# Kernel tuning notes

Measured on AMD Instinct MI355X. Metric: run time of the kernel, lower is better.

Reference implementation:

```python
import jax, jax.numpy as jnp
import numpy as np

B, T, D, H = 4, 2048, 1024, 16
DK = D // H

def setup_inputs() -> dict:
    key = jax.random.key(0)
    k1, k2, k3 = jax.random.split(key, 3)
    x = jax.random.normal(k1, (B, T, D), dtype=jnp.float32)
    w_qkv = jax.random.normal(k2, (D, 3 * D), dtype=jnp.float32) * (1.0 / np.sqrt(D))
    w_proj = jax.random.normal(k3, (D, D), dtype=jnp.float32) * (1.0 / np.sqrt(D))
    # additive causal mask: 0 on/below diagonal, -inf above
    neg = jnp.finfo(jnp.float32).min
    attn_mask = jnp.where(jnp.tril(jnp.ones((T, T), dtype=bool)), 0.0, neg)[None, None]
    return {"x": x, "attn_mask": attn_mask, "w_qkv": w_qkv, "w_proj": w_proj}


def reference(x, attn_mask, w_qkv, w_proj):
    Bx, Tx, Dx = x.shape
    qkv = x @ w_qkv                                  # [B,T,3D]
    q, k, v = jnp.split(qkv, 3, axis=-1)
    # [B,T,D] -> [B,H,T,dk]
    def to_heads(t):
        return t.reshape(Bx, Tx, H, DK).transpose(0, 2, 1, 3)
    q, k, v = to_heads(q), to_heads(k), to_heads(v)
    attn = jnp.einsum("bhqd,bhkd->bhqk", q, k) / jnp.sqrt(jnp.float32(DK))
    attn = attn + attn_mask
    attn = jax.nn.softmax(attn, axis=-1)
    out = jnp.einsum("bhqk,bhkd->bhqd", attn, v)     # [B,H,T,dk]
    out = out.transpose(0, 2, 1, 3).reshape(Bx, Tx, Dx)
    return out @ w_proj
```

## Files before the change

### kernel.cpp

```cpp
#include <hip/hip_runtime.h>
#include <hip/hip_bf16.h>
#include <stdint.h>

typedef __bf16 bf16x8 __attribute__((ext_vector_type(8)));
typedef __bf16 bf16x4 __attribute__((ext_vector_type(4)));
typedef float  f32x4  __attribute__((ext_vector_type(4)));

__device__ __forceinline__ void gl_lds16(const void* g, void* l) {
  __builtin_amdgcn_global_load_lds(
      (const __attribute__((address_space(1))) unsigned int*)g,
      (__attribute__((address_space(3))) unsigned int*)l, 16, 0, 0);
}

__global__ __launch_bounds__(256) void prep_kernel(
    const float* __restrict__ x, __bf16* __restrict__ Xb,
    const float* __restrict__ w_qkv, __bf16* __restrict__ wt_qkv,
    const float* __restrict__ w_proj, __bf16* __restrict__ wt_proj) {
  __shared__ __bf16 tile[64][65];
  const int bid = blockIdx.x, t = threadIdx.x;
  if (bid < 4096) {
    const size_t i = ((size_t)bid * 256 + t) * 8;
    float4 v0 = *reinterpret_cast<const float4*>(x + i);
    float4 v1 = *reinterpret_cast<const float4*>(x + i + 4);
    bf16x8 o;
    o[0] = (__bf16)v0.x; o[1] = (__bf16)v0.y; o[2] = (__bf16)v0.z; o[3] = (__bf16)v0.w;
    o[4] = (__bf16)v1.x; o[5] = (__bf16)v1.y; o[6] = (__bf16)v1.z; o[7] = (__bf16)v1.w;
    *reinterpret_cast<bf16x8*>(Xb + i) = o;
    return;
  }
  const float* src; __bf16* dst; int K, N, bx, by;
  if (bid < 4864) {
    int idx = bid - 4096;
    src = w_qkv; dst = wt_qkv; K = 1024; N = 3072;
    bx = idx % 48; by = idx / 48;
  } else {
    int idx = bid - 4864;
    src = w_proj; dst = wt_proj; K = 1024; N = 1024;
    bx = idx & 15; by = idx >> 4;
  }
  const int n0 = bx * 64, k0 = by * 64;
#pragma unroll
  for (int e = 0; e < 16; ++e) {
    int idx = e * 256 + t;
    int kk = idx >> 6, nn = idx & 63;
    tile[nn][kk] = (__bf16)src[(size_t)(k0 + kk) * N + n0 + nn];
  }
  __syncthreads();
#pragma unroll
  for (int e = 0; e < 16; ++e) {
    int idx = e * 256 + t;
    int nn = idx >> 6, kk = idx & 63;
    dst[(size_t)(n0 + nn) * K + k0 + kk] = tile[nn][kk];
  }
}

template <int NFRAG>
__device__ __forceinline__ void gemm_core_1024(
    const __bf16* __restrict__ Ag, const __bf16* __restrict__ Bg,
    int m0, int n0, __bf16* lds, f32x4 (&acc)[8][NFRAG]) {
  constexpr int BUFSZ = 4096 + NFRAG * 2048;
  const int tid = threadIdx.x;
  const int wv = tid >> 6, l = tid & 63, g = l >> 4, lr = l & 15;
  const int sswL = (lr & 3) ^ ((lr >> 2) & 3);

  int arow[2], acol[2], brow[NFRAG], bcol[NFRAG];
#pragma unroll
  for (int e = 0; e < 2; ++e) {
    int c = e * 256 + tid, row = c >> 2, slot = c & 3;
    arow[e] = row;
    acol[e] = (slot ^ ((row & 3) ^ ((row >> 2) & 3))) * 8;
  }
#pragma unroll
  for (int e = 0; e < NFRAG; ++e) {
    int c = e * 256 + tid, row = c >> 2, slot = c & 3;
    brow[e] = row;
    bcol[e] = (slot ^ ((row & 3) ^ ((row >> 2) & 3))) * 8;
  }

  auto STAGE = [&](int bufb, int t) {
    const int kb = t * 32;
#pragma unroll
    for (int e = 0; e < 2; ++e)
      gl_lds16(Ag + (size_t)(m0 + arow[e]) * 1024 + kb + acol[e],
               lds + bufb + (e * 256 + wv * 64) * 8);
#pragma unroll
    for (int e = 0; e < NFRAG; ++e)
      gl_lds16(Bg + (size_t)(n0 + brow[e]) * 1024 + kb + bcol[e],
               lds + bufb + 4096 + (e * 256 + wv * 64) * 8);
  };

  int cur = 0, nx = BUFSZ, nn = 2 * BUFSZ;
  STAGE(cur, 0);
  STAGE(nx, 1);

#pragma unroll 1
  for (int t = 0; t < 32; ++t) {
    if (t < 31) {
      if constexpr (NFRAG == 3) asm volatile("s_waitcnt vmcnt(5)" ::: "memory");
      else                      asm volatile("s_waitcnt vmcnt(4)" ::: "memory");
    } else {
      asm volatile("s_waitcnt vmcnt(0)" ::: "memory");
    }
    __builtin_amdgcn_s_barrier();
    __builtin_amdgcn_sched_barrier(0);
    if (t + 2 < 32) STAGE(nn, t + 2);

    const char* Ab = (const char*)(lds + cur);
    const char* Bb = (const char*)(lds + cur + 4096);
    bf16x8 a[8], b[NFRAG];
#pragma unroll
    for (int mf = 0; mf < 8; ++mf)
      a[mf] = *reinterpret_cast<const bf16x8*>(
          Ab + (mf * 16 + lr) * 64 + ((g ^ sswL) << 4));
#pragma unroll
    for (int nf = 0; nf < NFRAG; ++nf)
      b[nf] = *reinterpret_cast<const bf16x8*>(
          Bb + (wv * NFRAG * 16 + nf * 16 + lr) * 64 + ((g ^ sswL) << 4));
    __builtin_amdgcn_s_setprio(1);
#pragma unroll
    for (int mf = 0; mf < 8; ++mf)
#pragma unroll
      for (int nf = 0; nf < NFRAG; ++nf)
        acc[mf][nf] = __builtin_amdgcn_mfma_f32_16x16x32_bf16(
            a[mf], b[nf], acc[mf][nf], 0, 0, 0);
    __builtin_amdgcn_s_setprio(0);

    int tmp = cur; cur = nx; nx = nn; nn = tmp;
  }
}

__global__ __launch_bounds__(256, 2) void qkv_gemm(
    const __bf16* __restrict__ Xb, const __bf16* __restrict__ WT,
    __bf16* __restrict__ Qb, __bf16* __restrict__ Kb, __bf16* __restrict__ Vb) {
  __shared__ __bf16 lds[30720];
  const int lin = blockIdx.x;
  const int sw = (lin & 7) * 128 + (lin >> 3);
  const int rb = sw >> 4, cb = sw & 15;
  const int m0 = rb * 128, n0 = cb * 192;

  f32x4 acc[8][3] = {};
  gemm_core_1024<3>(Xb, WT, m0, n0, lds, acc);

  const int tid = threadIdx.x, wv = tid >> 6, l = tid & 63, g = l >> 4, lr = l & 15;
#pragma unroll
  for (int mf = 0; mf < 8; ++mf)
#pragma unroll
    for (int nf = 0; nf < 3; ++nf) {
      int m_ = m0 + mf * 16 + g * 4;
      int nb = n0 + wv * 48 + nf * 16;
      int which = nb >> 10, hc = nb & 1023;
      int hh = hc >> 6, dk0 = hc & 63;
      int bbv = m_ >> 11, tt = m_ & 2047;
      if (which == 2) {
        bf16x4 vk;
        vk[0] = (__bf16)acc[mf][nf][0]; vk[1] = (__bf16)acc[mf][nf][1];
        vk[2] = (__bf16)acc[mf][nf][2]; vk[3] = (__bf16)acc[mf][nf][3];
        *reinterpret_cast<bf16x4*>(
            &Vb[((size_t)(bbv * 16 + hh) * 64 + dk0 + lr) * 2048 + tt]) = vk;
      } else if (which == 0) {
#pragma unroll
        for (int j = 0; j < 4; ++j)
          Qb[(((size_t)(bbv * 16 + hh)) * 2048 + tt + j) * 64 + dk0 + lr] =
              (__bf16)(acc[mf][nf][j] * 0.18033688f);
      } else {
#pragma unroll
        for (int j = 0; j < 4; ++j)
          Kb[(((size_t)(bbv * 16 + hh)) * 2048 + tt + j) * 64 + dk0 + lr] =
              (__bf16)acc[mf][nf][j];
      }
    }
}

__global__ __launch_bounds__(256, 2) void proj_gemm(
    const __bf16* __restrict__ A, const __bf16* __restrict__ WT,
    float* __restrict__ Out) {
  __shared__ __bf16 lds[24576];
  const int lin = blockIdx.x;
  const int sw = (lin & 7) * 64 + (lin >> 3);
  const int rb = sw >> 3, cb = sw & 7;
  const int m0 = rb * 128, n0 = cb * 128;

  f32x4 acc[8][2] = {};
  gemm_core_1024<2>(A, WT, m0, n0, lds, acc);

  const int tid = threadIdx.x, wv = tid >> 6, l = tid & 63, g = l >> 4, lr = l & 15;
#pragma unroll
  for (int mf = 0; mf < 8; ++mf)
#pragma unroll
    for (int nf = 0; nf < 2; ++nf) {
      int m_ = m0 + mf * 16 + g * 4;
      int n  = n0 + wv * 32 + nf * 16 + lr;
#pragma unroll
      for (int j = 0; j < 4; ++j)
        Out[(size_t)(m_ + j) * 1024 + n] = acc[mf][nf][j];
    }
}

__global__ __launch_bounds__(256, 2) void attn_kernel(
    const __bf16* __restrict__ Qb, const __bf16* __restrict__ Kb,
    const __bf16* __restrict__ VTb, __bf16* __restrict__ Ob) {
  __shared__ __bf16 Ks[2][4096];
  __shared__ __bf16 Vs[2][4096];
  __shared__ __bf16 PlA[4][1024];
  __shared__ __bf16 PlB[4][1024];
  const int t = threadIdx.x, l = t & 63, w = t >> 6;
  const int g = l >> 4, lr = l & 15;
  const int bid = blockIdx.x;
  const int logical = (bid & 7) * 64 + (bid >> 3);
  const int pj = logical & 7, bh = logical >> 3;
  const int bb = bh >> 4, h = bh & 15;
  const __bf16* Kbase = Kb  + (size_t)bh * 2048 * 64;
  const __bf16* Vbase = VTb + (size_t)bh * 64 * 2048;
  const __bf16* Qbase = Qb  + (size_t)bh * 2048 * 64;
  const int swz = (lr & 7) << 4;

  int cur = 0;
#pragma unroll 1
  for (int phase = 0; phase < 2; ++phase) {
    const int J = phase ? (15 - pj) : pj;
    const int qtA = 2 * J, qtB = 2 * J + 1;
    const int qrowA = J * 128 + w * 16 + lr;
    const int qrowB = qrowA + 64;
    const bf16x8 qfA0 = *reinterpret_cast<const bf16x8*>(Qbase + (size_t)qrowA * 64 + g * 8);
    const bf16x8 qfA1 = *reinterpret_cast<const bf16x8*>(Qbase + (size_t)qrowA * 64 + 32 + g * 8);
    const bf16x8 qfB0 = *reinterpret_cast<const bf16x8*>(Qbase + (size_t)qrowB * 64 + g * 8);
    const bf16x8 qfB1 = *reinterpret_cast<const bf16x8*>(Qbase + (size_t)qrowB * 64 + 32 + g * 8);

    f32x4 otA[4] = {}, otB[4] = {};
    float lsA = 0.f, lsB = 0.f;

#pragma unroll
    for (int rep = 0; rep < 2; ++rep) {
      int c = w * 128 + rep * 64 + l;
      int row = c >> 3, cc = c & 7;
      int pc = (cc ^ (row & 7)) * 8;
      gl_lds16(Kbase + (size_t)row * 64 + pc, &Ks[cur][(w * 128 + rep * 64) * 8]);
      gl_lds16(Vbase + (size_t)row * 2048 + pc, &Vs[cur][(w * 128 + rep * 64) * 8]);
    }
    __syncthreads();

    for (int kt = 0; kt <= qtB; ++kt) {
      const bool aAct = (kt <= qtA);
      if (kt < qtB) {
        const int nv0 = (kt + 1) * 64;
#pragma unroll
        for (int rep = 0; rep < 2; ++rep) {
          int c = w * 128 + rep * 64 + l;
          int row = c >> 3, cc = c & 7;
          int pc = (cc ^ (row & 7)) * 8;
          gl_lds16(Kbase + (size_t)(nv0 + row) * 64 + pc,
                   &Ks[cur ^ 1][(w * 128 + rep * 64) * 8]);
          gl_lds16(Vbase + (size_t)row * 2048 + nv0 + pc,
                   &Vs[cur ^ 1][(w * 128 + rep * 64) * 8]);
        }
      }
      bf16x8 klo[4], khi[4];
#pragma unroll
      for (int nf = 0; nf < 4; ++nf) {
        const char* kr = (const char*)&Ks[cur][(nf * 16 + lr) * 64];
        klo[nf] = *reinterpret_cast<const bf16x8*>(kr + ((g * 16) ^ swz));
        khi[nf] = *reinterpret_cast<const bf16x8*>(kr + ((64 + g * 16) ^ swz));
      }
      f32x4 stA[4], stB[4];
      __builtin_amdgcn_s_setprio(1);
#pragma unroll
      for (int nf = 0; nf < 4; ++nf) {
        f32x4 z = {};
        z = __builtin_amdgcn_mfma_f32_16x16x32_bf16(klo[nf], qfB0, z, 0, 0, 0);
        stB[nf] = __builtin_amdgcn_mfma_f32_16x16x32_bf16(khi[nf], qfB1, z, 0, 0, 0);
      }
      if (aAct) {
#pragma unroll
        for (int nf = 0; nf < 4; ++nf) {
          f32x4 z = {};
          z = __builtin_amdgcn_mfma_f32_16x16x32_bf16(klo[nf], qfA0, z, 0, 0, 0);
          stA[nf] = __builtin_amdgcn_mfma_f32_16x16x32_bf16(khi[nf], qfA1, z, 0, 0, 0);
        }
      }
      __builtin_amdgcn_s_setprio(0);
      if (kt == qtB) {
#pragma unroll
        for (int nf = 0; nf < 4; ++nf)
#pragma unroll
          for (int j = 0; j < 4; ++j)
            if (nf * 16 + g * 4 + j > w * 16 + lr) stB[nf][j] = -INFINITY;
      }
      if (aAct && kt == qtA) {
#pragma unroll
        for (int nf = 0; nf < 4; ++nf)
#pragma unroll
          for (int j = 0; j < 4; ++j)
            if (nf * 16 + g * 4 + j > w * 16 + lr) stA[nf][j] = -INFINITY;
      }
      {
        float rs = 0.f;
        char* prow = (char*)&PlB[w][lr * 64];
#pragma unroll
        for (int nf = 0; nf < 4; ++nf) {
#pragma unroll
          for (int j = 0; j < 4; ++j) {
            float p = __builtin_amdgcn_exp2f(stB[nf][j]);
            stB[nf][j] = p;
            rs += p;
          }
          bf16x4 pk;
          pk[0] = (__bf16)stB[nf][0]; pk[1] = (__bf16)stB[nf][1];
          pk[2] = (__bf16)stB[nf][2]; pk[3] = (__bf16)stB[nf][3];
          *reinterpret_cast<bf16x4*>(prow + ((nf * 32 + g * 8) ^ swz)) = pk;
        }
        lsB += rs;
      }
      if (aAct) {
        float rs = 0.f;
        char* prow = (char*)&PlA[w][lr * 64];
#pragma unroll
        for (int nf = 0; nf < 4; ++nf) {
#pragma unroll
          for (int j = 0; j < 4; ++j) {
            float p = __builtin_amdgcn_exp2f(stA[nf][j]);
            stA[nf][j] = p;
            rs += p;
          }
          bf16x4 pk;
          pk[0] = (__bf16)stA[nf][0]; pk[1] = (__bf16)stA[nf][1];
          pk[2] = (__bf16)stA[nf][2]; pk[3] = (__bf16)stA[nf][3];
          *reinterpret_cast<bf16x4*>(prow + ((nf * 32 + g * 8) ^ swz)) = pk;
        }
        lsA += rs;
      }
      {
        bf16x8 vlo[4], vhi[4];
#pragma unroll
        for (int nf = 0; nf < 4; ++nf) {
          const char* vr = (const char*)&Vs[cur][(nf * 16 + lr) * 64];
          vlo[nf] = *reinterpret_cast<const bf16x8*>(vr + ((g * 16) ^ swz));
          vhi[nf] = *reinterpret_cast<const bf16x8*>(vr + ((64 + g * 16) ^ swz));
        }
        const char* prB = (const char*)&PlB[w][lr * 64];
        bf16x8 pb0 = *reinterpret_cast<const bf16x8*>(prB + ((g * 16) ^ swz));
        bf16x8 pb1 = *reinterpret_cast<const bf16x8*>(prB + ((64 + g * 16) ^ swz));
        __builtin_amdgcn_s_setprio(1);
#pragma unroll
        for (int nf = 0; nf < 4; ++nf) {
          otB[nf] = __builtin_amdgcn_mfma_f32_16x16x32_bf16(vlo[nf], pb0, otB[nf], 0, 0, 0);
          otB[nf] = __builtin_amdgcn_mfma_f32_16x16x32_bf16(vhi[nf], pb1, otB[nf], 0, 0, 0);
        }
        __builtin_amdgcn_s_setprio(0);
        if (aAct) {
          const char* prA = (const char*)&PlA[w][lr * 64];
          bf16x8 pa0 = *reinterpret_cast<const bf16x8*>(prA + ((g * 16) ^ swz));
          bf16x8 pa1 = *reinterpret_cast<const bf16x8*>(prA + ((64 + g * 16) ^ swz));
          __builtin_amdgcn_s_setprio(1);
#pragma unroll
          for (int nf = 0; nf < 4; ++nf) {
            otA[nf] = __builtin_amdgcn_mfma_f32_16x16x32_bf16(vlo[nf], pa0, otA[nf], 0, 0, 0);
            otA[nf] = __builtin_amdgcn_mfma_f32_16x16x32_bf16(vhi[nf], pa1, otA[nf], 0, 0, 0);
          }
          __builtin_amdgcn_s_setprio(0);
        }
      }
      __syncthreads();
      cur ^= 1;
    }

    lsA += __shfl_xor(lsA, 16); lsA += __shfl_xor(lsA, 32);
    lsB += __shfl_xor(lsB, 16); lsB += __shfl_xor(lsB, 32);
    const float rlA = 1.f / lsA, rlB = 1.f / lsB;
#pragma unroll
    for (int nf = 0; nf < 4; ++nf) {
      bf16x4 ok;
      ok[0] = (__bf16)(otA[nf][0] * rlA); ok[1] = (__bf16)(otA[nf][1] * rlA);
      ok[2] = (__bf16)(otA[nf][2] * rlA); ok[3] = (__bf16)(otA[nf][3] * rlA);
      *reinterpret_cast<bf16x4*>(
          &Ob[((size_t)(bb * 2048 + qrowA)) * 1024 + h * 64 + nf * 16 + g * 4]) = ok;
      bf16x4 ok2;
      ok2[0] = (__bf16)(otB[nf][0] * rlB); ok2[1] = (__bf16)(otB[nf][1] * rlB);
      ok2[2] = (__bf16)(otB[nf][2] * rlB); ok2[3] = (__bf16)(otB[nf][3] * rlB);
      *reinterpret_cast<bf16x4*>(
          &Ob[((size_t)(bb * 2048 + qrowB)) * 1024 + h * 64 + nf * 16 + g * 4]) = ok2;
    }
  }
}

extern "C" void kernel_launch(void* const* d_in, const int* in_sizes, int n_in,
                              void* d_out, int out_size, void* d_ws, size_t ws_size,
                              hipStream_t stream) {
  const float* x      = (const float*)d_in[0];
  const float* w_qkv  = (const float*)d_in[2];
  const float* w_proj = (const float*)d_in[3];
  float* out = (float*)d_out;

  char* ws = (char*)d_ws;
  __bf16* wt_qkv  = (__bf16*)(ws);
  __bf16* wt_proj = (__bf16*)(ws + 6291456);
  __bf16* Qb      = (__bf16*)(ws + 8388608);
  __bf16* Kb      = (__bf16*)(ws + 8388608 + 16777216);
  __bf16* VTb     = (__bf16*)(ws + 8388608 + 2 * 16777216);
  __bf16* Ob      = (__bf16*)(ws + 8388608 + 3 * 16777216);
  __bf16* Xb      = Ob;

  prep_kernel<<<5120, 256, 0, stream>>>(x, Xb, w_qkv, wt_qkv, w_proj, wt_proj);
  qkv_gemm<<<1024, 256, 0, stream>>>(Xb, wt_qkv, Qb, Kb, VTb);
  attn_kernel<<<512, 256, 0, stream>>>(Qb, Kb, VTb, Ob);
  proj_gemm<<<512, 256, 0, stream>>>(Ob, wt_proj, out);
}
```

Baseline: 159.6 us.

## Switch attention to 32x32x16 MFMA and keep P in registers via lane shuffles

Rewrites the attention inner loop so each wave owns 32 query rows and uses 32x32x16 bf16 MFMA tiles instead of 16x16x32, which removes the split into A/B query halves. The softmax probabilities are repacked in registers with cross-half lane shuffles to form the B operand of the PV matmul, so the LDS round-trip and the P shared buffers are gone. It also drops the per-half inactive-tile skipping, so some fully masked work in the diagonal tile is now computed. Register pressure rises with the 16-wide accumulators.

```diff
diff --git a/kernel.cpp b/kernel.cpp
--- a/kernel.cpp
+++ b/kernel.cpp
@@ -5,11 +5,18 @@
 typedef __bf16 bf16x8 __attribute__((ext_vector_type(8)));
 typedef __bf16 bf16x4 __attribute__((ext_vector_type(4)));
 typedef float  f32x4  __attribute__((ext_vector_type(4)));
+typedef float  f32x16 __attribute__((ext_vector_type(16)));
 
 __device__ __forceinline__ void gl_lds16(const void* g, void* l) {
   __builtin_amdgcn_global_load_lds(
       (const __attribute__((address_space(1))) unsigned int*)g,
       (__attribute__((address_space(3))) unsigned int*)l, 16, 0, 0);
+}
+
+__device__ __forceinline__ unsigned pk2(float a, float b) {
+  union { __bf16 h[2]; unsigned u; } z;
+  z.h[0] = (__bf16)a; z.h[1] = (__bf16)b;
+  return z.u;
 }
 
 __global__ __launch_bounds__(256) void prep_kernel(
@@ -201,10 +208,8 @@
     const __bf16* __restrict__ VTb, __bf16* __restrict__ Ob) {
   __shared__ __bf16 Ks[2][4096];
   __shared__ __bf16 Vs[2][4096];
-  __shared__ __bf16 PlA[4][1024];
-  __shared__ __bf16 PlB[4][1024];
   const int t = threadIdx.x, l = t & 63, w = t >> 6;
-  const int g = l >> 4, lr = l & 15;
+  const int q5 = l & 31, hi = l >> 5;
   const int bid = blockIdx.x;
   const int logical = (bid & 7) * 64 + (bid >> 3);
   const int pj = logical & 7, bh = logical >> 3;
@@ -212,173 +217,140 @@
   const __bf16* Kbase = Kb  + (size_t)bh * 2048 * 64;
   const __bf16* Vbase = VTb + (size_t)bh * 64 * 2048;
   const __bf16* Qbase = Qb  + (size_t)bh * 2048 * 64;
-  const int swz = (lr & 7) << 4;
+
+  auto STAGEKV = [&](int buf, int kt) {
+#pragma unroll
+    for (int rep = 0; rep < 2; ++rep) {
+      int c = w * 128 + rep * 64 + l;
+      int row = c >> 3, cc = c & 7;
+      int pc = (cc ^ (row & 7)) * 8;
+      gl_lds16(Kbase + (size_t)(kt * 64 + row) * 64 + pc,
+               &Ks[buf][(w * 128 + rep * 64) * 8]);
+      gl_lds16(Vbase + (size_t)row * 2048 + kt * 64 + pc,
+               &Vs[buf][(w * 128 + rep * 64) * 8]);
+    }
+  };
 
   int cur = 0;
 #pragma unroll 1
   for (int phase = 0; phase < 2; ++phase) {
     const int J = phase ? (15 - pj) : pj;
-    const int qtA = 2 * J, qtB = 2 * J + 1;
-    const int qrowA = J * 128 + w * 16 + lr;
-    const int qrowB = qrowA + 64;
-    const bf16x8 qfA0 = *reinterpret_cast<const bf16x8*>(Qbase + (size_t)qrowA * 64 + g * 8);
-    const bf16x8 qfA1 = *reinterpret_cast<const bf16x8*>(Qbase + (size_t)qrowA * 64 + 32 + g * 8);
-    const bf16x8 qfB0 = *reinterpret_cast<const bf16x8*>(Qbase + (size_t)qrowB * 64 + g * 8);
-    const bf16x8 qfB1 = *reinterpret_cast<const bf16x8*>(Qbase + (size_t)qrowB * 64 + 32 + g * 8);
-
-    f32x4 otA[4] = {}, otB[4] = {};
-    float lsA = 0.f, lsB = 0.f;
-
-#pragma unroll
-    for (int rep = 0; rep < 2; ++rep) {
-      int c = w * 128 + rep * 64 + l;
-      int row = c >> 3, cc = c & 7;
-      int pc = (cc ^ (row & 7)) * 8;
-      gl_lds16(Kbase + (size_t)row * 64 + pc, &Ks[cur][(w * 128 + rep * 64) * 8]);
-      gl_lds16(Vbase + (size_t)row * 2048 + pc, &Vs[cur][(w * 128 + rep * 64) * 8]);
-    }
+    const int qloc = w * 32 + q5;
+    const int qrow = J * 128 + qloc;
+
+    bf16x8 qf[4];
+#pragma unroll
+    for (int ks = 0; ks < 4; ++ks)
+      qf[ks] = *reinterpret_cast<const bf16x8*>(
+          Qbase + (size_t)qrow * 64 + ks * 16 + hi * 8);
+
+    f32x16 ot[2] = {};
+    float lsum = 0.f;
+
+    STAGEKV(cur, 0);
     __syncthreads();
 
-    for (int kt = 0; kt <= qtB; ++kt) {
-      const bool aAct = (kt <= qtA);
-      if (kt < qtB) {
-        const int nv0 = (kt + 1) * 64;
-#pragma unroll
-        for (int rep = 0; rep < 2; ++rep) {
-          int c = w * 128 + rep * 64 + l;
-          int row = c >> 3, cc = c & 7;
-          int pc = (cc ^ (row & 7)) * 8;
-          gl_lds16(Kbase + (size_t)(nv0 + row) * 64 + pc,
-                   &Ks[cur ^ 1][(w * 128 + rep * 64) * 8]);
-          gl_lds16(Vbase + (size_t)row * 2048 + nv0 + pc,
-                   &Vs[cur ^ 1][(w * 128 + rep * 64) * 8]);
-        }
-      }
-      bf16x8 klo[4], khi[4];
-#pragma unroll
-      for (int nf = 0; nf < 4; ++nf) {
-        const char* kr = (const char*)&Ks[cur][(nf * 16 + lr) * 64];
-        klo[nf] = *reinterpret_cast<const bf16x8*>(kr + ((g * 16) ^ swz));
-        khi[nf] = *reinterpret_cast<const bf16x8*>(kr + ((64 + g * 16) ^ swz));
-      }
-      f32x4 stA[4], stB[4];
-      __builtin_amdgcn_s_setprio(1);
-#pragma unroll
-      for (int nf = 0; nf < 4; ++nf) {
-        f32x4 z = {};
-        z = __builtin_amdgcn_mfma_f32_16x16x32_bf16(klo[nf], qfB0, z, 0, 0, 0);
-        stB[nf] = __builtin_amdgcn_mfma_f32_16x16x32_bf16(khi[nf], qfB1, z, 0, 0, 0);
-      }
-      if (aAct) {
-#pragma unroll
-        for (int nf = 0; nf < 4; ++nf) {
-          f32x4 z = {};
-          z = __builtin_amdgcn_mfma_f32_16x16x32_bf16(klo[nf], qfA0, z, 0, 0, 0);
-          stA[nf] = __builtin_amdgcn_mfma_f32_16x16x32_bf16(khi[nf], qfA1, z, 0, 0, 0);
-        }
-      }
-      __builtin_amdgcn_s_setprio(0);
-      if (kt == qtB) {
-#pragma unroll
-        for (int nf = 0; nf < 4; ++nf)
-#pragma unroll
-          for (int j = 0; j < 4; ++j)
-            if (nf * 16 + g * 4 + j > w * 16 + lr) stB[nf][j] = -INFINITY;
-      }
-      if (aAct && kt == qtA) {
-#pragma unroll
-        for (int nf = 0; nf < 4; ++nf)
-#pragma unroll
-          for (int j = 0; j < 4; ++j)
-            if (nf * 16 + g * 4 + j > w * 16 + lr) stA[nf][j] = -INFINITY;
-      }
+    const int NT = 2 * J + 2;
+    for (int kt = 0; kt < NT; ++kt) {
+      if (kt + 1 < NT) STAGEKV(cur ^ 1, kt + 1);
+
+      f32x16 s[2] = {};
       {
-        float rs = 0.f;
-        char* prow = (char*)&PlB[w][lr * 64];
-#pragma unroll
-        for (int nf = 0; nf < 4; ++nf) {
-#pragma unroll
-          for (int j = 0; j < 4; ++j) {
-            float p = __builtin_amdgcn_exp2f(stB[nf][j]);
-            stB[nf][j] = p;
-            rs += p;
-          }
-          bf16x4 pk;
-          pk[0] = (__bf16)stB[nf][0]; pk[1] = (__bf16)stB[nf][1];
-          pk[2] = (__bf16)stB[nf][2]; pk[3] = (__bf16)stB[nf][3];
-          *reinterpret_cast<bf16x4*>(prow + ((nf * 32 + g * 8) ^ swz)) = pk;
-        }
-        lsB += rs;
-      }
-      if (aAct) {
-        float rs = 0.f;
-        char* prow = (char*)&PlA[w][lr * 64];
-#pragma unroll
-        for (int nf = 0; nf < 4; ++nf) {
-#pragma unroll
-          for (int j = 0; j < 4; ++j) {
-            float p = __builtin_amdgcn_exp2f(stA[nf][j]);
-            stA[nf][j] = p;
-            rs += p;
-          }
-          bf16x4 pk;
-          pk[0] = (__bf16)stA[nf][0]; pk[1] = (__bf16)stA[nf][1];
-          pk[2] = (__bf16)stA[nf][2]; pk[3] = (__bf16)stA[nf][3];
-          *reinterpret_cast<bf16x4*>(prow + ((nf * 32 + g * 8) ^ swz)) = pk;
-        }
-        lsA += rs;
-      }
+        const char* kr0 = (const char*)&Ks[cur][q5 * 64];
+        const char* kr1 = (const char*)&Ks[cur][(32 + q5) * 64];
+        const int sz = (q5 & 7) << 4;
+        __builtin_amdgcn_s_setprio(1);
+#pragma unroll
+        for (int ks = 0; ks < 4; ++ks) {
+          bf16x8 kf0 = *reinterpret_cast<const bf16x8*>(kr0 + ((ks * 32 + hi * 16) ^ sz));
+          bf16x8 kf1 = *reinterpret_cast<const bf16x8*>(kr1 + ((ks * 32 + hi * 16) ^ sz));
+          s[0] = __builtin_amdgcn_mfma_f32_32x32x16_bf16(kf0, qf[ks], s[0], 0, 0, 0);
+          s[1] = __builtin_amdgcn_mfma_f32_32x32x16_bf16(kf1, qf[ks], s[1], 0, 0, 0);
+        }
+        __builtin_amdgcn_s_setprio(0);
+      }
+
+      if (kt >= 2 * J) {
+        const int doff = (kt - 2 * J) * 64;
+#pragma unroll
+        for (int r = 0; r < 16; ++r) {
+          int kvloc = (r & 3) + 8 * (r >> 2) + 4 * hi;
+          if (doff + kvloc > qloc)      s[0][r] = -INFINITY;
+          if (doff + 32 + kvloc > qloc) s[1][r] = -INFINITY;
+        }
+      }
+      float rs = 0.f;
+#pragma unroll
+      for (int kvb = 0; kvb < 2; ++kvb)
+#pragma unroll
+        for (int r = 0; r < 16; ++r) {
+          float p = __builtin_amdgcn_exp2f(s[kvb][r]);
+          s[kvb][r] = p;
+          rs += p;
+        }
+      lsum += rs;
+
+      bf16x8 pb[4];
+#pragma unroll
+      for (int k = 0; k < 4; ++k) {
+        const int rb = (k & 1) * 8;
+        float o0, o1, o2, o3, e0, e1, e2, e3;
+        if (k < 2) {
+          o0 = s[0][rb + 4 * hi + 0]; o1 = s[0][rb + 4 * hi + 1];
+          o2 = s[0][rb + 4 * hi + 2]; o3 = s[0][rb + 4 * hi + 3];
+          e0 = s[0][rb + 4 * (1 - hi) + 0]; e1 = s[0][rb + 4 * (1 - hi) + 1];
+          e2 = s[0][rb + 4 * (1 - hi) + 2]; e3 = s[0][rb + 4 * (1 - hi) + 3];
+        } else {
+          o0 = s[1][rb + 4 * hi + 0]; o1 = s[1][rb + 4 * hi + 1];
+          o2 = s[1][rb + 4 * hi + 2]; o3 = s[1][rb + 4 * hi + 3];
+          e0 = s[1][rb + 4 * (1 - hi) + 0]; e1 = s[1][rb + 4 * (1 - hi) + 1];
+          e2 = s[1][rb + 4 * (1 - hi) + 2]; e3 = s[1][rb + 4 * (1 - hi) + 3];
+        }
+        unsigned ownA = pk2(o0, o1), ownB = pk2(o2, o3);
+        unsigned sndA = pk2(e0, e1), sndB = pk2(e2, e3);
+        unsigned gA = (unsigned)__shfl_xor((int)sndA, 32);
+        unsigned gB = (unsigned)__shfl_xor((int)sndB, 32);
+        union { unsigned u[4]; bf16x8 v; } z;
+        z.u[0] = hi ? gA : ownA;
+        z.u[1] = hi ? gB : ownB;
+        z.u[2] = hi ? ownA : gA;
+        z.u[3] = hi ? ownB : gB;
+        pb[k] = z.v;
+      }
+
       {
-        bf16x8 vlo[4], vhi[4];
-#pragma unroll
-        for (int nf = 0; nf < 4; ++nf) {
-          const char* vr = (const char*)&Vs[cur][(nf * 16 + lr) * 64];
-          vlo[nf] = *reinterpret_cast<const bf16x8*>(vr + ((g * 16) ^ swz));
-          vhi[nf] = *reinterpret_cast<const bf16x8*>(vr + ((64 + g * 16) ^ swz));
-        }
-        const char* prB = (const char*)&PlB[w][lr * 64];
-        bf16x8 pb0 = *reinterpret_cast<const bf16x8*>(prB + ((g * 16) ^ swz));
-        bf16x8 pb1 = *reinterpret_cast<const bf16x8*>(prB + ((64 + g * 16) ^ swz));
+        const char* vr0 = (const char*)&Vs[cur][q5 * 64];
+        const char* vr1 = (const char*)&Vs[cur][(32 + q5) * 64];
+        const int sz = (q5 & 7) << 4;
         __builtin_amdgcn_s_setprio(1);
 #pragma unroll
-        for (int nf = 0; nf < 4; ++nf) {
-          otB[nf] = __builtin_amdgcn_mfma_f32_16x16x32_bf16(vlo[nf], pb0, otB[nf], 0, 0, 0);
-          otB[nf] = __builtin_amdgcn_mfma_f32_16x16x32_bf16(vhi[nf], pb1, otB[nf], 0, 0, 0);
+        for (int ks = 0; ks < 4; ++ks) {
+          bf16x8 vf0 = *reinterpret_cast<const bf16x8*>(vr0 + ((ks * 32 + hi * 16) ^ sz));
+          bf16x8 vf1 = *reinterpret_cast<const bf16x8*>(vr1 + ((ks * 32 + hi * 16) ^ sz));
+          ot[0] = __builtin_amdgcn_mfma_f32_32x32x16_bf16(vf0, pb[ks], ot[0], 0, 0, 0);
+          ot[1] = __builtin_amdgcn_mfma_f32_32x32x16_bf16(vf1, pb[ks], ot[1], 0, 0, 0);
         }
         __builtin_amdgcn_s_setprio(0);
-        if (aAct) {
-          const char* prA = (const char*)&PlA[w][lr * 64];
-          bf16x8 pa0 = *reinterpret_cast<const bf16x8*>(prA + ((g * 16) ^ swz));
-          bf16x8 pa1 = *reinterpret_cast<const bf16x8*>(prA + ((64 + g * 16) ^ swz));
-          __builtin_amdgcn_s_setprio(1);
-#pragma unroll
-          for (int nf = 0; nf < 4; ++nf) {
-            otA[nf] = __builtin_amdgcn_mfma_f32_16x16x32_bf16(vlo[nf], pa0, otA[nf], 0, 0, 0);
-            otA[nf] = __builtin_amdgcn_mfma_f32_16x16x32_bf16(vhi[nf], pa1, otA[nf], 0, 0, 0);
-          }
-          __builtin_amdgcn_s_setprio(0);
-        }
       }
       __syncthreads();
       cur ^= 1;
     }
 
-    lsA += __shfl_xor(lsA, 16); lsA += __shfl_xor(lsA, 32);
-    lsB += __shfl_xor(lsB, 16); lsB += __shfl_xor(lsB, 32);
-    const float rlA = 1.f / lsA, rlB = 1.f / lsB;
-#pragma unroll
-    for (int nf = 0; nf < 4; ++nf) {
-      bf16x4 ok;
-      ok[0] = (__bf16)(otA[nf][0] * rlA); ok[1] = (__bf16)(otA[nf][1] * rlA);
-      ok[2] = (__bf16)(otA[nf][2] * rlA); ok[3] = (__bf16)(otA[nf][3] * rlA);
-      *reinterpret_cast<bf16x4*>(
-          &Ob[((size_t)(bb * 2048 + qrowA)) * 1024 + h * 64 + nf * 16 + g * 4]) = ok;
-      bf16x4 ok2;
-      ok2[0] = (__bf16)(otB[nf][0] * rlB); ok2[1] = (__bf16)(otB[nf][1] * rlB);
-      ok2[2] = (__bf16)(otB[nf][2] * rlB); ok2[3] = (__bf16)(otB[nf][3] * rlB);
-      *reinterpret_cast<bf16x4*>(
-          &Ob[((size_t)(bb * 2048 + qrowB)) * 1024 + h * 64 + nf * 16 + g * 4]) = ok2;
-    }
+    lsum += __shfl_xor(lsum, 32);
+    const float rl = 1.f / lsum;
+#pragma unroll
+    for (int dkb = 0; dkb < 2; ++dkb)
+#pragma unroll
+      for (int rq = 0; rq < 4; ++rq) {
+        bf16x4 ok;
+        ok[0] = (__bf16)(ot[dkb][rq * 4 + 0] * rl);
+        ok[1] = (__bf16)(ot[dkb][rq * 4 + 1] * rl);
+        ok[2] = (__bf16)(ot[dkb][rq * 4 + 2] * rl);
+        ok[3] = (__bf16)(ot[dkb][rq * 4 + 3] * rl);
+        int dk = dkb * 32 + rq * 8 + 4 * hi;
+        *reinterpret_cast<bf16x4*>(
+            &Ob[((size_t)(bb * 2048 + qrow)) * 1024 + h * 64 + dk]) = ok;
+      }
   }
 }
 
```

Result: slower. 250.3 us (+56.8%).
